# Performance work log

Measured on AMD Instinct MI355X. Metric: run time of the kernel, lower is better.

The kernel has to match this reference:

```python
import jax, jax.numpy as jnp
import numpy as np

N_NODES = 50000
N_EDGES = 800000
IN_CH = 128
HIDDEN = 64
LATENT = 64
OUT_CH = 128
N_GRAPHS = 500
NEG_SLOPE = 0.2


def _gat_layer(x, src, dst, W, a_src, a_dst, b, n_nodes):
    """PyG GATConv (heads=1, concat=True, add_self_loops=True, edge_dim=None)."""
    h = x @ W  # [N, F]
    loops = jnp.arange(n_nodes)
    s = jnp.concatenate([src, loops])  # source (j) of each edge incl. self loops
    d = jnp.concatenate([dst, loops])  # destination (i)
    score_src = h @ a_src  # [N]
    score_dst = h @ a_dst  # [N]
    alpha = jax.nn.leaky_relu(score_src[s] + score_dst[d], NEG_SLOPE)  # [E+N]
    # softmax grouped by destination node
    amax = jax.ops.segment_max(alpha, d, num_segments=n_nodes)
    e = jnp.exp(alpha - amax[d])
    denom = jax.ops.segment_sum(e, d, num_segments=n_nodes)
    coef = e / (denom[d] + 1e-16)
    out = jax.ops.segment_sum(h[s] * coef[:, None], d, num_segments=n_nodes)
    return out + b


def setup_inputs() -> dict:
    key = jax.random.key(0)
    ks = jax.random.split(key, 24)
    g = lambda k, shape, fan: jax.random.normal(k, shape, jnp.float32) * (1.0 / np.sqrt(fan))
    inp = {
        "x": jax.random.normal(ks[0], (N_NODES, IN_CH), jnp.float32),
        "edge_index": jax.random.randint(ks[1], (2, N_EDGES), 0, N_NODES, dtype=jnp.int64),
        "batch": jnp.sort(jax.random.randint(ks[2], (N_NODES,), 0, N_GRAPHS, dtype=jnp.int64)),
        "edge_attr": jax.random.normal(ks[3], (N_EDGES, 3), jnp.float32),
        # conv1 (GATConv in->hidden)
        "W1": g(ks[4], (IN_CH, HIDDEN), IN_CH),
        "a_src1": g(ks[5], (HIDDEN,), HIDDEN),
        "a_dst1": g(ks[6], (HIDDEN,), HIDDEN),
        "b1": jnp.zeros((HIDDEN,), jnp.float32),
        # conv2 (GATConv hidden->latent)
        "W2": g(ks[7], (HIDDEN, LATENT), HIDDEN),
        "a_src2": g(ks[8], (LATENT,), LATENT),
        "a_dst2": g(ks[9], (LATENT,), LATENT),
        "b2": jnp.zeros((LATENT,), jnp.float32),
        # encoder linear
        "lin_W": g(ks[10], (LATENT, LATENT), LATENT),
        "lin_b": jnp.zeros((LATENT,), jnp.float32),
        # decoder x_mlp
        "xm_W1": g(ks[11], (LATENT, HIDDEN), LATENT),
        "xm_b1": jnp.zeros((HIDDEN,), jnp.float32),
        "xm_W2": g(ks[12], (HIDDEN, OUT_CH), HIDDEN),
        "xm_b2": jnp.zeros((OUT_CH,), jnp.float32),
        # decoder edge_mlp
        "em_W1": g(ks[13], (LATENT, HIDDEN), LATENT),
        "em_b1": jnp.zeros((HIDDEN,), jnp.float32),
        "em_W2": g(ks[14], (HIDDEN, 3), HIDDEN),
        "em_b2": jnp.zeros((3,), jnp.float32),
    }
    return inp


def reference(x, edge_index, batch, edge_attr,
              W1, a_src1, a_dst1, b1,
              W2, a_src2, a_dst2, b2,
              lin_W, lin_b,
              xm_W1, xm_b1, xm_W2, xm_b2,
              em_W1, em_b1, em_W2, em_b2):
    src, dst = edge_index[0], edge_index[1]
    n = x.shape[0]
    # Encoder (eval mode: dropout is identity; edge_attr unused since edge_dim=None)
    h = _gat_layer(x, src, dst, W1, a_src1, a_dst1, b1, n)
    h = jax.nn.relu(h)
    z = _gat_layer(h, src, dst, W2, a_src2, a_dst2, b2, n)
    z = z @ lin_W + lin_b
    # global_mean_pool over batch ids
    sums = jax.ops.segment_sum(z, batch, num_segments=N_GRAPHS)
    counts = jax.ops.segment_sum(jnp.ones((n,), z.dtype), batch, num_segments=N_GRAPHS)
    graph_embedding = sums / jnp.maximum(counts, 1.0)[:, None]
    # MLP decoders
    x_hat = jax.nn.relu(z @ xm_W1 + xm_b1) @ xm_W2 + xm_b2
    e_hat = jax.nn.relu(z @ em_W1 + em_b1) @ em_W2 + em_b2
    return (x_hat, e_hat, z, graph_embedding)
```

## Files before the change

kernel.cpp:

```cpp
#include <hip/hip_runtime.h>
#include <hip/hip_bf16.h>
#include <cstring>

#define N_NODES 50000
#define N_EDGES 800000
#define IN_CH 128
#define NG 500
#define OUT_ELEMS 9782000
#define NBUCK 196
#define GEMMB 3125
#define DECB 3125

using bf16 = __hip_bfloat16;
typedef unsigned short u16;
typedef unsigned int u32;
typedef long long i64;
typedef unsigned long long u64;

__device__ __forceinline__ float b2f(bf16 v) { return __bfloat162float(v); }
__device__ __forceinline__ float tofl(float v) { return v; }
__device__ __forceinline__ float tofl(bf16 v) { return __bfloat162float(v); }
__device__ __forceinline__ float ldflt(const void* p, int i, int f32) {
  return f32 ? ((const float*)p)[i] : b2f(((const bf16*)p)[i]);
}
__device__ __forceinline__ int ldedge(const void* p, int i, int is64) {
  return is64 ? (int)((const i64*)p)[i] : ((const int*)p)[i];
}
__device__ __forceinline__ float sane(float v) {
  if (!isfinite(v)) return 0.f;
  return fminf(fmaxf(v, -65504.f), 65504.f);
}
__device__ __forceinline__ float lrelu(float x) { return x > 0.f ? x : 0.2f * x; }
__device__ __forceinline__ float bflo(u32 u) { return __uint_as_float(u << 16); }
__device__ __forceinline__ float bfhi(u32 u) { return __uint_as_float(u & 0xffff0000u); }

__device__ __forceinline__ float wsum(float v) {
#pragma unroll
  for (int o = 32; o > 0; o >>= 1) v += __shfl_xor(v, o, 64);
  return v;
}


__global__ void fillsig_kernel(float* __restrict__ out, int n, float v) {
  int i = blockIdx.x * 256 + threadIdx.x;
  if (i < n) out[i] = v;
}

#define BCHUNK 4096

__global__ __launch_bounds__(256) void hist196_kernel(const void* __restrict__ ei,
                                                      const u16* __restrict__ xb,
                                                      int* __restrict__ bpart,
                                                      int* __restrict__ fl) {
  int bid = blockIdx.x, tid = threadIdx.x;
  __shared__ int cs;
  __shared__ int hist[NBUCK];
  if (bid < NBUCK) {
    if (tid == 0) cs = 0;
    if (tid < NBUCK) hist[tid] = 0;
    __syncthreads();
    const int* e32 = (const int*)ei;
    atomicAdd(&cs, (e32[2 * tid + 1] == 0) ? 1 : 0);
    __syncthreads();
    int is64 = cs > 128;
    int base = bid * BCHUNK;
#pragma unroll
    for (int k = 0; k < 16; ++k) {
      int e = base + k * 256 + tid;
      if (e < N_EDGES) {
        unsigned d = (unsigned)ldedge(ei, N_EDGES + e, is64);
        if (d < N_NODES) atomicAdd(&hist[d >> 8], 1);
      }
    }
    __syncthreads();
    if (tid < NBUCK) bpart[bid * 256 + tid] = hist[tid];
    return;
  }
  if (tid == 0) cs = 0;
  __syncthreads();
  int cnt = 0;
  if (bid == NBUCK) {
#pragma unroll 4
    for (int k = 0; k < 32; ++k) {
      int i = tid + 256 * k;
      u16 u = xb[2 * i];
      int e = (u >> 7) & 0xFF;
      if (e != 0 && (e < 90 || e > 150)) ++cnt;
    }
  } else {
    const int* e32 = (const int*)ei;
#pragma unroll 4
    for (int k = 0; k < 32; ++k) {
      int i = tid + 256 * k;
      if (e32[2 * i + 1] == 0) ++cnt;
    }
  }
  atomicAdd(&cs, cnt);
  __syncthreads();
  if (tid == 0) fl[bid == NBUCK ? 7 : 6] = cs;
}

__global__ __launch_bounds__(256) void scan196_kernel(const int* __restrict__ bpart,
                                                      int* __restrict__ bcur,
                                                      int* __restrict__ bstart,
                                                      int* __restrict__ offs) {
  __shared__ int sm[256];
  int t = threadIdx.x;
  int sum = 0;
  if (t < NBUCK)
    for (int b = 0; b < NBUCK; ++b) sum += bpart[b * 256 + t];
  sm[t] = (t < NBUCK) ? sum : 0;
  __syncthreads();
  for (int off = 1; off < 256; off <<= 1) {
    int add = (t >= off) ? sm[t - off] : 0;
    __syncthreads();
    sm[t] += add;
    __syncthreads();
  }
  if (t < NBUCK) {
    int start = sm[t] - sum;
    bcur[t] = start;
    bstart[t] = start;
  }
  if (t == 255) {
    bstart[NBUCK] = sm[255];
    offs[N_NODES] = sm[255];
  }
}

template <int FIN, typename FT>
__device__ void gemm16_compute(float (&xl)[16][FIN], const void* Wv, const void* asv,
                               const void* adv, bf16* __restrict__ h, float* __restrict__ ss,
                               float* __restrict__ sd, int rbase) {
  const FT* W = (const FT*)Wv;
  const FT* as_ = (const FT*)asv;
  const FT* ad_ = (const FT*)adv;
  int lane = threadIdx.x & 63, w = threadIdx.x >> 6;
  float a_s = tofl(as_[lane]), a_d = tofl(ad_[lane]);
  int r0 = w * 4;
  float acc0 = 0.f, acc1 = 0.f, acc2 = 0.f, acc3 = 0.f;
  for (int k = 0; k < FIN; ++k) {
    float wk = tofl(W[k * 64 + lane]);
    acc0 = fmaf(xl[r0 + 0][k], wk, acc0);
    acc1 = fmaf(xl[r0 + 1][k], wk, acc1);
    acc2 = fmaf(xl[r0 + 2][k], wk, acc2);
    acc3 = fmaf(xl[r0 + 3][k], wk, acc3);
  }
  float acc[4] = {sane(acc0), sane(acc1), sane(acc2), sane(acc3)};
#pragma unroll
  for (int j = 0; j < 4; ++j) {
    int g = rbase + r0 + j;
    h[g * 64 + lane] = __float2bfloat16(acc[j]);
    float vs = wsum(acc[j] * a_s);
    float vd = wsum(acc[j] * a_d);
    if (lane == 0) { ss[g] = sane(vs); sd[g] = sane(vd); }
  }
}

__global__ __launch_bounds__(256) void bucket_gemm_kernel(
    const void* __restrict__ ei, int* __restrict__ bcur, u64* __restrict__ tmp,
    const void* __restrict__ xin, const void* __restrict__ W, const void* __restrict__ asrc,
    const void* __restrict__ adst, const int* __restrict__ fl, bf16* __restrict__ h,
    float* __restrict__ ss, float* __restrict__ sd) {
  __shared__ int hist[NBUCK], run[NBUCK], gbase[NBUCK];
  __shared__ float xl[16][IN_CH];
  int bid = blockIdx.x, tid = threadIdx.x;
  int is64 = fl[6] > 4000;
  int wf = fl[7] > 2000;
  if (bid < NBUCK) {
    if (tid < NBUCK) { hist[tid] = 0; run[tid] = 0; }
    __syncthreads();
    int base = bid * BCHUNK;
#pragma unroll
    for (int k = 0; k < 16; ++k) {
      int e = base + k * 256 + tid;
      if (e < N_EDGES) {
        unsigned d = (unsigned)ldedge(ei, N_EDGES + e, is64);
        if (d < N_NODES) atomicAdd(&hist[d >> 8], 1);
      }
    }
    __syncthreads();
    if (tid < NBUCK) {
      int hh = hist[tid];
      gbase[tid] = hh ? atomicAdd(&bcur[tid], hh) : 0;
    }
    __syncthreads();
#pragma unroll
    for (int k = 0; k < 16; ++k) {
      int e = base + k * 256 + tid;
      if (e < N_EDGES) {
        unsigned d = (unsigned)ldedge(ei, N_EDGES + e, is64);
        if (d < N_NODES) {
          unsigned s = (unsigned)ldedge(ei, e, is64);
          if (s >= N_NODES) s = 0;
          int pos = gbase[d >> 8] + atomicAdd(&run[d >> 8], 1);
          if ((unsigned)pos < N_EDGES) tmp[pos] = ((u64)s << 32) | (u64)d;
        }
      }
    }
    return;
  }
  int rbase = (bid - NBUCK) * 16;
  for (int i = tid; i < 16 * IN_CH; i += 256) {
    int rr = i / IN_CH, cc = i % IN_CH;
    xl[rr][cc] = ldflt(xin, (rbase + rr) * IN_CH + cc, wf);
  }
  __syncthreads();
  if (wf)
    gemm16_compute<IN_CH, float>(xl, W, asrc, adst, h, ss, sd, rbase);
  else
    gemm16_compute<IN_CH, bf16>(xl, W, asrc, adst, h, ss, sd, rbase);
}

__global__ __launch_bounds__(1024) void scatter2b_kernel(const u64* __restrict__ tmp,
                                                         const int* __restrict__ bstart,
                                                         int* __restrict__ offs,
                                                         int* __restrict__ csr) {
  __shared__ int lcnt[256], lex[256], lcur[256];
  int b = blockIdx.x;
  int tid = threadIdx.x;
  if (tid < 256) { lcnt[tid] = 0; lcur[tid] = 0; }
  __syncthreads();
  int nodelo = b << 8;
  int beg = bstart[b], end = bstart[b + 1];
  beg = max(0, min(beg, N_EDGES));
  end = max(beg, min(end, N_EDGES));
  for (int i = beg + tid; i < end; i += 1024) {
    int d = (int)(tmp[i] & 0xFFFFFFFFu);
    unsigned li = (unsigned)(d - nodelo);
    if (li < 256) atomicAdd(&lcnt[li], 1);
  }
  __syncthreads();
  if (tid < 256) lex[tid] = lcnt[tid];
  __syncthreads();
  for (int off = 1; off < 256; off <<= 1) {
    int add = (tid < 256 && tid >= off) ? lex[tid - off] : 0;
    __syncthreads();
    if (tid < 256) lex[tid] += add;
    __syncthreads();
  }
  if (tid < 256) {
    int ex = lex[tid] - lcnt[tid];
    lex[tid] = ex;
    int node = nodelo + tid;
    if (node < N_NODES) offs[node] = beg + ex;
  }
  __syncthreads();
  for (int i = beg + tid; i < end; i += 1024) {
    u64 v = tmp[i];
    int d = (int)(v & 0xFFFFFFFFu);
    int s = (int)(v >> 32);
    unsigned li = (unsigned)(d - nodelo);
    if (li < 256) {
      int pos = beg + lex[li] + atomicAdd(&lcur[li], 1);
      if ((unsigned)pos < N_EDGES) csr[pos] = s;
    }
  }
}

__device__ __forceinline__ float2 agg_node2(const bf16* __restrict__ h,
                                            const float* __restrict__ ss,
                                            const float* __restrict__ sd,
                                            const int* __restrict__ offs,
                                            const int* __restrict__ csr, int d, int lane) {
  int hl = lane & 31;
  int hbase = lane & 32;
  float sdd = sd[d];
  int beg = offs[d], end = offs[d + 1];
  beg = max(0, min(beg, N_EDGES));
  end = max(beg, min(end, N_EDGES));
  float wself = __expf(fminf(lrelu(ss[d] + sdd), 60.f));
  u32 uself = ((const u32*)h)[d * 32 + hl];
  float2 acc;
  acc.x = bflo(uself) * wself;
  acc.y = bfhi(uself) * wself;
  float dpart = (hl == 0) ? wself : 0.f;
  for (int cb = beg; cb < end; cb += 32) {
    int j = cb + hl;
    int s = 0;
    float wv = 0.f;
    if (j < end) {
      s = csr[j];
      s = ((unsigned)s < N_NODES) ? s : 0;
      wv = __expf(fminf(lrelu(ss[s] + sdd), 60.f));
    }
    dpart += wv;
    int cnt = min(32, end - cb);
    for (int t0 = 0; t0 < cnt; t0 += 16) {
      u32 hv[16];
#pragma unroll
      for (int q = 0; q < 16; ++q) {
        int sq = __shfl(s, hbase + t0 + q, 64);
        hv[q] = ((const u32*)h)[sq * 32 + hl];
      }
#pragma unroll
      for (int q = 0; q < 16; ++q) {
        float wq = __shfl(wv, hbase + t0 + q, 64);
        acc.x = fmaf(bflo(hv[q]), wq, acc.x);
        acc.y = fmaf(bfhi(hv[q]), wq, acc.y);
      }
    }
  }
#pragma unroll
  for (int o = 16; o > 0; o >>= 1) dpart += __shfl_xor(dpart, o, 64);
  float den = dpart + 1e-16f;
  acc.x = acc.x / den;
  acc.y = acc.y / den;
  return acc;
}

template <typename FT>
__device__ void gemm2_compute(float (&xl)[8][64], int r0, const void* Wv, const void* asv,
                              const void* adv, bf16* __restrict__ h, float* __restrict__ ss,
                              float* __restrict__ sd, int rbase) {
  const FT* W = (const FT*)Wv;
  const FT* as_ = (const FT*)asv;
  const FT* ad_ = (const FT*)adv;
  int lane = threadIdx.x & 63;
  float a_s = tofl(as_[lane]), a_d = tofl(ad_[lane]);
  float acc0 = 0.f, acc1 = 0.f;
  for (int k = 0; k < 64; ++k) {
    float wk = tofl(W[k * 64 + lane]);
    acc0 = fmaf(xl[r0 + 0][k], wk, acc0);
    acc1 = fmaf(xl[r0 + 1][k], wk, acc1);
  }
  float acc[2] = {sane(acc0), sane(acc1)};
#pragma unroll
  for (int j = 0; j < 2; ++j) {
    int g = rbase + r0 + j;
    h[g * 64 + lane] = __float2bfloat16(acc[j]);
    float vs = wsum(acc[j] * a_s);
    float vd = wsum(acc[j] * a_d);
    if (lane == 0) { ss[g] = sane(vs); sd[g] = sane(vd); }
  }
}

template <typename FT>
__device__ void lin2_compute(float (&xl)[8][64], int r0, const void* Wv, const void* bv,
                             float* __restrict__ zio, int rbase) {
  const FT* W = (const FT*)Wv;
  const FT* b = (const FT*)bv;
  int lane = threadIdx.x & 63;
  float bl = tofl(b[lane]);
  float acc0 = bl, acc1 = bl;
  for (int k = 0; k < 64; ++k) {
    float wk = tofl(W[k * 64 + lane]);
    acc0 = fmaf(xl[r0 + 0][k], wk, acc0);
    acc1 = fmaf(xl[r0 + 1][k], wk, acc1);
  }
  float acc[2] = {sane(acc0), sane(acc1)};
#pragma unroll
  for (int j = 0; j < 2; ++j) zio[(rbase + r0 + j) * 64 + lane] = acc[j];
}

__global__ __launch_bounds__(256) void agg_gemm_kernel(
    const bf16* __restrict__ hL, const float* __restrict__ ssL, const float* __restrict__ sdL,
    const int* __restrict__ offs, const int* __restrict__ csr, const void* __restrict__ bias,
    const int* __restrict__ fl, const void* __restrict__ W2, const void* __restrict__ as2,
    const void* __restrict__ ad2, bf16* __restrict__ hOut, float* __restrict__ ssOut,
    float* __restrict__ sdOut) {
  __shared__ float o1l[8][64];
  int wf = fl[7] > 2000;
  int lane = threadIdx.x & 63, w = threadIdx.x >> 6;
  int hl = lane & 31, half = lane >> 5;
  int rbase = blockIdx.x * 8;
  int d = rbase + 2 * w + half;
  float2 r = agg_node2(hL, ssL, sdL, offs, csr, d, lane);
  float blx = ldflt(bias, 2 * hl, wf), bly = ldflt(bias, 2 * hl + 1, wf);
  o1l[2 * w + half][2 * hl] = sane(fmaxf(r.x + blx, 0.f));
  o1l[2 * w + half][2 * hl + 1] = sane(fmaxf(r.y + bly, 0.f));
  __syncthreads();
  if (wf)
    gemm2_compute<float>(o1l, 2 * w, W2, as2, ad2, hOut, ssOut, sdOut, rbase);
  else
    gemm2_compute<bf16>(o1l, 2 * w, W2, as2, ad2, hOut, ssOut, sdOut, rbase);
}

__global__ __launch_bounds__(256) void agg_lin_kernel(
    const bf16* __restrict__ hL, const float* __restrict__ ssL, const float* __restrict__ sdL,
    const int* __restrict__ offs, const int* __restrict__ csr, const void* __restrict__ bias,
    const int* __restrict__ fl, const void* __restrict__ linW, const void* __restrict__ linb,
    float* __restrict__ zreg) {
  __shared__ float o2l[8][64];
  int wf = fl[7] > 2000;
  int lane = threadIdx.x & 63, w = threadIdx.x >> 6;
  int hl = lane & 31, half = lane >> 5;
  int rbase = blockIdx.x * 8;
  int d = rbase + 2 * w + half;
  float2 r = agg_node2(hL, ssL, sdL, offs, csr, d, lane);
  float blx = ldflt(bias, 2 * hl, wf), bly = ldflt(bias, 2 * hl + 1, wf);
  o2l[2 * w + half][2 * hl] = sane(r.x + blx);
  o2l[2 * w + half][2 * hl + 1] = sane(r.y + bly);
  __syncthreads();
  if (wf)
    lin2_compute<float>(o2l, 2 * w, linW, linb, zreg, rbase);
  else
    lin2_compute<bf16>(o2l, 2 * w, linW, linb, zreg, rbase);
}

template <typename FT>
__device__ void dec16_compute(float (&zl)[16][64], float (&t1x)[16][64], float (&t1e)[16][65],
                              float (&W2l)[192], const void* xW1v, const void* xb1v,
                              const void* xW2v, const void* xb2v, const void* eW1v,
                              const void* eb1v, const void* eb2v, float* __restrict__ xout,
                              float* __restrict__ eout, int rbase) {
  const FT* xW1 = (const FT*)xW1v;
  const FT* xb1 = (const FT*)xb1v;
  const FT* xW2 = (const FT*)xW2v;
  const FT* xb2 = (const FT*)xb2v;
  const FT* eW1 = (const FT*)eW1v;
  const FT* eb1 = (const FT*)eb1v;
  const FT* eb2 = (const FT*)eb2v;
  int lane = threadIdx.x & 63, w = threadIdx.x >> 6;
  int r0 = w * 4;
  {
    float bx = tofl(xb1[lane]), be = tofl(eb1[lane]);
    float x0 = bx, x1 = bx, x2 = bx, x3 = bx;
    float e0 = be, e1 = be, e2 = be, e3 = be;
    for (int k = 0; k < 64; ++k) {
      float z0 = zl[r0 + 0][k], z1 = zl[r0 + 1][k];
      float z2 = zl[r0 + 2][k], z3 = zl[r0 + 3][k];
      float wx = tofl(xW1[k * 64 + lane]);
      float we = tofl(eW1[k * 64 + lane]);
      x0 = fmaf(z0, wx, x0);
      x1 = fmaf(z1, wx, x1);
      x2 = fmaf(z2, wx, x2);
      x3 = fmaf(z3, wx, x3);
      e0 = fmaf(z0, we, e0);
      e1 = fmaf(z1, we, e1);
      e2 = fmaf(z2, we, e2);
      e3 = fmaf(z3, we, e3);
    }
    t1x[r0 + 0][lane] = fmaxf(x0, 0.f);
    t1x[r0 + 1][lane] = fmaxf(x1, 0.f);
    t1x[r0 + 2][lane] = fmaxf(x2, 0.f);
    t1x[r0 + 3][lane] = fmaxf(x3, 0.f);
    t1e[r0 + 0][lane] = fmaxf(e0, 0.f);
    t1e[r0 + 1][lane] = fmaxf(e1, 0.f);
    t1e[r0 + 2][lane] = fmaxf(e2, 0.f);
    t1e[r0 + 3][lane] = fmaxf(e3, 0.f);
  }
  {
    float b2a = tofl(xb2[lane]), b2b = tofl(xb2[64 + lane]);
    float a0[4] = {b2a, b2a, b2a, b2a};
    float a1[4] = {b2b, b2b, b2b, b2b};
    for (int k = 0; k < 64; ++k) {
      float wa = tofl(xW2[k * 128 + lane]);
      float wb = tofl(xW2[k * 128 + 64 + lane]);
#pragma unroll
      for (int j = 0; j < 4; ++j) {
        float tv = t1x[r0 + j][k];
        a0[j] = fmaf(tv, wa, a0[j]);
        a1[j] = fmaf(tv, wb, a1[j]);
      }
    }
#pragma unroll
    for (int j = 0; j < 4; ++j) {
      int g = rbase + r0 + j;
      xout[g * 128 + lane] = sane(a0[j]);
      xout[g * 128 + 64 + lane] = sane(a1[j]);
    }
  }
  {
    int j = lane >> 4, c = lane & 15;
    if (c < 3) {
      int row = r0 + j;
      float acc = tofl(eb2[c]);
#pragma unroll 4
      for (int k = 0; k < 64; ++k) acc = fmaf(t1e[row][k], W2l[k * 3 + c], acc);
      eout[(rbase + row) * 3 + c] = sane(acc);
    }
  }
}

__global__ __launch_bounds__(256) void dec_pool_kernel(
    const float* __restrict__ z, const void* __restrict__ xmW1, const void* __restrict__ xmb1,
    const void* __restrict__ xmW2, const void* __restrict__ xmb2, const void* __restrict__ emW1,
    const void* __restrict__ emb1, const void* __restrict__ emW2, const void* __restrict__ emb2,
    const void* __restrict__ batch, const int* __restrict__ fl, float* __restrict__ xout,
    float* __restrict__ eout, float* __restrict__ emb) {
  __shared__ float zl[16][64];
  __shared__ float t1x[16][64];
  __shared__ float t1e[16][65];
  __shared__ float W2l[192];
  int tid = threadIdx.x;
  if (blockIdx.x < NG) {
    float(&sm)[4][64] = *reinterpret_cast<float(*)[4][64]>(&zl[0][0]);
    int* bounds = (int*)&t1x[0][0];
    int g = blockIdx.x;
    int lane = tid & 63, w = tid >> 6;
    int is64 = fl[6] > 4000;
    if (tid < 2) {
      int target = g + tid;
      int lo = 0, hi = N_NODES;
      while (lo < hi) {
        int mid = (lo + hi) >> 1;
        if (ldedge(batch, mid, is64) < target) lo = mid + 1; else hi = mid;
      }
      bounds[tid] = lo;
    }
    __syncthreads();
    int beg = bounds[0], end = bounds[1];
    float acc = 0.f;
    for (int r = beg + w; r < end; r += 4) acc += z[r * 64 + lane];
    sm[w][lane] = acc;
    __syncthreads();
    if (w == 0) {
      float v = sm[0][lane] + sm[1][lane] + sm[2][lane] + sm[3][lane];
      float cnt = (float)max(end - beg, 1);
      emb[g * 64 + lane] = sane(v / cnt);
    }
    return;
  }
  int wf = fl[7] > 2000;
  int rbase = (blockIdx.x - NG) * 16;
  for (int i = tid; i < 1024; i += 256) zl[i >> 6][i & 63] = z[rbase * 64 + i];
  if (tid < 192) W2l[tid] = wf ? ((const float*)emW2)[tid] : b2f(((const bf16*)emW2)[tid]);
  __syncthreads();
  if (wf)
    dec16_compute<float>(zl, t1x, t1e, W2l, xmW1, xmb1, xmW2, xmb2, emW1, emb1, emb2,
                         xout, eout, rbase);
  else
    dec16_compute<bf16>(zl, t1x, t1e, W2l, xmW1, xmb1, xmW2, xmb2, emW1, emb1, emb2,
                        xout, eout, rbase);
}

extern "C" void kernel_launch(void* const* d_in, const int* in_sizes, int n_in,
                              void* d_out, int out_size, void* d_ws, size_t ws_size,
                              hipStream_t stream) {
  float* outf = (float*)d_out;
  if (out_size != OUT_ELEMS) {
    float sig = 2048.0f + fminf((float)out_size * 1e-4f, 999.f);
    fillsig_kernel<<<(out_size + 255) / 256, 256, 0, stream>>>(outf, out_size, sig);
    return;
  }
  if (n_in < 22 || in_sizes[0] != N_NODES * IN_CH || in_sizes[1] != 2 * N_EDGES) {
    fillsig_kernel<<<(out_size + 255) / 256, 256, 0, stream>>>(outf, out_size, 5000.f);
    return;
  }

  const void* x = d_in[0];
  const void* ei = d_in[1];
  const void* batch = d_in[2];
  const void* W1 = d_in[4];
  const void* as1 = d_in[5];
  const void* ad1 = d_in[6];
  const void* b1 = d_in[7];
  const void* W2 = d_in[8];
  const void* as2 = d_in[9];
  const void* ad2 = d_in[10];
  const void* b2 = d_in[11];
  const void* linW = d_in[12];
  const void* linb = d_in[13];
  const void* xmW1 = d_in[14];
  const void* xmb1 = d_in[15];
  const void* xmW2 = d_in[16];
  const void* xmb2 = d_in[17];
  const void* emW1 = d_in[18];
  const void* emb1 = d_in[19];
  const void* emW2 = d_in[20];
  const void* emb2 = d_in[21];

  float* xhat = outf;
  float* ehat = outf + 6400000;
  float* zreg = outf + 6550000;
  float* emb = outf + 9750000;

  bool usews = ws_size >= (size_t)17100000;
  char* base = usews ? (char*)d_ws : (char*)d_out;
  int* bpart = (int*)(base + 0);
  int* offs = (int*)(base + 400000);
  int* bcur = (int*)(base + 600016);
  int* bstart = (int*)(base + 600816);
  int* flags = (int*)(base + 601616);
  float* ssb = (float*)(base + 601728);
  float* sdb = (float*)(base + 801728);
  int* csr = (int*)(base + 1001728);
  bf16* hbuf = (bf16*)(base + 4201728);
  u64* tmp = (u64*)(base + 10601728);
  float* ss2 = (float*)(base + 0);
  float* sd2 = (float*)(base + 200000);
  bf16* hbuf2 = (bf16*)(base + 10601728);

  int err = 0, idx = 0;
  (void)hipGetLastError();
#define CK()                                                                       \
  do {                                                                             \
    ++idx;                                                                         \
    hipError_t e_ = hipGetLastError();                                             \
    if (e_ != hipSuccess && err == 0) err = 8192 + idx * 256 + ((int)e_ & 3) * 64; \
  } while (0)

  hist196_kernel<<<NBUCK + 2, 256, 0, stream>>>(ei, (const u16*)x, bpart, flags); CK();
  scan196_kernel<<<1, 256, 0, stream>>>(bpart, bcur, bstart, offs); CK();
  bucket_gemm_kernel<<<NBUCK + GEMMB, 256, 0, stream>>>(
      ei, bcur, tmp, x, W1, as1, ad1, flags, hbuf, ssb, sdb); CK();
  scatter2b_kernel<<<NBUCK, 1024, 0, stream>>>(tmp, bstart, offs, csr); CK();
  agg_gemm_kernel<<<N_NODES / 8, 256, 0, stream>>>(hbuf, ssb, sdb, offs, csr, b1, flags,
                                                   W2, as2, ad2, hbuf2, ss2, sd2); CK();
  agg_lin_kernel<<<N_NODES / 8, 256, 0, stream>>>(hbuf2, ss2, sd2, offs, csr, b2, flags,
                                                  linW, linb, zreg); CK();
  dec_pool_kernel<<<NG + DECB, 256, 0, stream>>>(zreg, xmW1, xmb1, xmW2, xmb2,
                                                 emW1, emb1, emW2, emb2, batch, flags,
                                                 xhat, ehat, emb); CK();
#undef CK

  if (err != 0) {
    static float s_sent;
    s_sent = (float)err;
    (void)hipMemcpyAsync(d_out, &s_sent, 4, hipMemcpyHostToDevice, stream);
  }
}
```

Before: 305.7 us.

## Replace histogram+scan CSR build with fixed-capacity bucket slots and packed edges

Removes the separate histogram and prefix-scan kernels by giving each destination bucket a fixed-capacity region (BCAP slots), so bucketing only needs an atomic counter per bucket, and folds the dtype-detection flags into the bucket/GEMM kernel. Edge entries are packed into 32-bit words (source shifted by 8, low destination byte) instead of 64-bit pairs, halving temp traffic. The CSR becomes padded per bucket, with explicit per-node end offsets used by the aggregation kernels. This drops two launches and one full edge pass. The cost is a larger workspace and silent truncation if any bucket exceeds its capacity.

```diff
diff --git a/kernel.cpp b/kernel.cpp
--- a/kernel.cpp
+++ b/kernel.cpp
@@ -8,6 +8,8 @@
 #define NG 500
 #define OUT_ELEMS 9782000
 #define NBUCK 196
+#define BCAP 8192
+#define CSRCAP (NBUCK * BCAP)
 #define GEMMB 3125
 #define DECB 3125
 
@@ -46,87 +48,12 @@
   if (i < n) out[i] = v;
 }
 
+__global__ void zero_kernel(int* __restrict__ p, int n) {
+  int i = threadIdx.x;
+  if (i < n) p[i] = 0;
+}
+
 #define BCHUNK 4096
-
-__global__ __launch_bounds__(256) void hist196_kernel(const void* __restrict__ ei,
-                                                      const u16* __restrict__ xb,
-                                                      int* __restrict__ bpart,
-                                                      int* __restrict__ fl) {
-  int bid = blockIdx.x, tid = threadIdx.x;
-  __shared__ int cs;
-  __shared__ int hist[NBUCK];
-  if (bid < NBUCK) {
-    if (tid == 0) cs = 0;
-    if (tid < NBUCK) hist[tid] = 0;
-    __syncthreads();
-    const int* e32 = (const int*)ei;
-    atomicAdd(&cs, (e32[2 * tid + 1] == 0) ? 1 : 0);
-    __syncthreads();
-    int is64 = cs > 128;
-    int base = bid * BCHUNK;
-#pragma unroll
-    for (int k = 0; k < 16; ++k) {
-      int e = base + k * 256 + tid;
-      if (e < N_EDGES) {
-        unsigned d = (unsigned)ldedge(ei, N_EDGES + e, is64);
-        if (d < N_NODES) atomicAdd(&hist[d >> 8], 1);
-      }
-    }
-    __syncthreads();
-    if (tid < NBUCK) bpart[bid * 256 + tid] = hist[tid];
-    return;
-  }
-  if (tid == 0) cs = 0;
-  __syncthreads();
-  int cnt = 0;
-  if (bid == NBUCK) {
-#pragma unroll 4
-    for (int k = 0; k < 32; ++k) {
-      int i = tid + 256 * k;
-      u16 u = xb[2 * i];
-      int e = (u >> 7) & 0xFF;
-      if (e != 0 && (e < 90 || e > 150)) ++cnt;
-    }
-  } else {
-    const int* e32 = (const int*)ei;
-#pragma unroll 4
-    for (int k = 0; k < 32; ++k) {
-      int i = tid + 256 * k;
-      if (e32[2 * i + 1] == 0) ++cnt;
-    }
-  }
-  atomicAdd(&cs, cnt);
-  __syncthreads();
-  if (tid == 0) fl[bid == NBUCK ? 7 : 6] = cs;
-}
-
-__global__ __launch_bounds__(256) void scan196_kernel(const int* __restrict__ bpart,
-                                                      int* __restrict__ bcur,
-                                                      int* __restrict__ bstart,
-                                                      int* __restrict__ offs) {
-  __shared__ int sm[256];
-  int t = threadIdx.x;
-  int sum = 0;
-  if (t < NBUCK)
-    for (int b = 0; b < NBUCK; ++b) sum += bpart[b * 256 + t];
-  sm[t] = (t < NBUCK) ? sum : 0;
-  __syncthreads();
-  for (int off = 1; off < 256; off <<= 1) {
-    int add = (t >= off) ? sm[t - off] : 0;
-    __syncthreads();
-    sm[t] += add;
-    __syncthreads();
-  }
-  if (t < NBUCK) {
-    int start = sm[t] - sum;
-    bcur[t] = start;
-    bstart[t] = start;
-  }
-  if (t == 255) {
-    bstart[NBUCK] = sm[255];
-    offs[N_NODES] = sm[255];
-  }
-}
 
 template <int FIN, typename FT>
 __device__ void gemm16_compute(float (&xl)[16][FIN], const void* Wv, const void* asv,
@@ -158,18 +85,22 @@
 }
 
 __global__ __launch_bounds__(256) void bucket_gemm_kernel(
-    const void* __restrict__ ei, int* __restrict__ bcur, u64* __restrict__ tmp,
+    const void* __restrict__ ei, int* __restrict__ bcnt, u32* __restrict__ tmp,
     const void* __restrict__ xin, const void* __restrict__ W, const void* __restrict__ asrc,
-    const void* __restrict__ adst, const int* __restrict__ fl, bf16* __restrict__ h,
+    const void* __restrict__ adst, int* __restrict__ fl, bf16* __restrict__ h,
     float* __restrict__ ss, float* __restrict__ sd) {
   __shared__ int hist[NBUCK], run[NBUCK], gbase[NBUCK];
   __shared__ float xl[16][IN_CH];
+  __shared__ int cs;
   int bid = blockIdx.x, tid = threadIdx.x;
-  int is64 = fl[6] > 4000;
-  int wf = fl[7] > 2000;
   if (bid < NBUCK) {
+    if (tid == 0) cs = 0;
     if (tid < NBUCK) { hist[tid] = 0; run[tid] = 0; }
     __syncthreads();
+    const int* e32 = (const int*)ei;
+    atomicAdd(&cs, (e32[2 * tid + 1] == 0) ? 1 : 0);
+    __syncthreads();
+    int is64 = cs > 128;
     int base = bid * BCHUNK;
 #pragma unroll
     for (int k = 0; k < 16; ++k) {
@@ -182,7 +113,7 @@
     __syncthreads();
     if (tid < NBUCK) {
       int hh = hist[tid];
-      gbase[tid] = hh ? atomicAdd(&bcur[tid], hh) : 0;
+      gbase[tid] = hh ? atomicAdd(&bcnt[tid], hh) : 0;
     }
     __syncthreads();
 #pragma unroll
@@ -193,14 +124,51 @@
         if (d < N_NODES) {
           unsigned s = (unsigned)ldedge(ei, e, is64);
           if (s >= N_NODES) s = 0;
-          int pos = gbase[d >> 8] + atomicAdd(&run[d >> 8], 1);
-          if ((unsigned)pos < N_EDGES) tmp[pos] = ((u64)s << 32) | (u64)d;
+          int t = d >> 8;
+          int pl = gbase[t] + atomicAdd(&run[t], 1);
+          if (pl < BCAP) tmp[t * BCAP + pl] = (s << 8) | (d & 255u);
         }
       }
     }
     return;
   }
-  int rbase = (bid - NBUCK) * 16;
+  if (bid < NBUCK + 2) {
+    if (tid == 0) cs = 0;
+    __syncthreads();
+    int cnt = 0;
+    if (bid == NBUCK) {
+      const u16* xb = (const u16*)xin;
+#pragma unroll 4
+      for (int k = 0; k < 32; ++k) {
+        int i = tid + 256 * k;
+        u16 u = xb[2 * i];
+        int e = (u >> 7) & 0xFF;
+        if (e != 0 && (e < 90 || e > 150)) ++cnt;
+      }
+    } else {
+      const int* e32 = (const int*)ei;
+#pragma unroll 4
+      for (int k = 0; k < 32; ++k) {
+        int i = tid + 256 * k;
+        if (e32[2 * i + 1] == 0) ++cnt;
+      }
+    }
+    atomicAdd(&cs, cnt);
+    __syncthreads();
+    if (tid == 0) fl[bid == NBUCK ? 7 : 6] = cs;
+    return;
+  }
+  if (tid == 0) cs = 0;
+  __syncthreads();
+  {
+    const u16* xb = (const u16*)xin;
+    u16 u = xb[2 * tid];
+    int e = (u >> 7) & 0xFF;
+    atomicAdd(&cs, (e != 0 && (e < 90 || e > 150)) ? 1 : 0);
+  }
+  __syncthreads();
+  int wf = cs > 64;
+  int rbase = (bid - NBUCK - 2) * 16;
   for (int i = tid; i < 16 * IN_CH; i += 256) {
     int rr = i / IN_CH, cc = i % IN_CH;
     xl[rr][cc] = ldflt(xin, (rbase + rr) * IN_CH + cc, wf);
@@ -212,9 +180,10 @@
     gemm16_compute<IN_CH, bf16>(xl, W, asrc, adst, h, ss, sd, rbase);
 }
 
-__global__ __launch_bounds__(1024) void scatter2b_kernel(const u64* __restrict__ tmp,
-                                                         const int* __restrict__ bstart,
+__global__ __launch_bounds__(1024) void scatter2c_kernel(const u32* __restrict__ tmp,
+                                                         const int* __restrict__ bcnt,
                                                          int* __restrict__ offs,
+                                                         int* __restrict__ ends,
                                                          int* __restrict__ csr) {
   __shared__ int lcnt[256], lex[256], lcur[256];
   int b = blockIdx.x;
@@ -222,13 +191,11 @@
   if (tid < 256) { lcnt[tid] = 0; lcur[tid] = 0; }
   __syncthreads();
   int nodelo = b << 8;
-  int beg = bstart[b], end = bstart[b + 1];
-  beg = max(0, min(beg, N_EDGES));
-  end = max(beg, min(end, N_EDGES));
-  for (int i = beg + tid; i < end; i += 1024) {
-    int d = (int)(tmp[i] & 0xFFFFFFFFu);
-    unsigned li = (unsigned)(d - nodelo);
-    if (li < 256) atomicAdd(&lcnt[li], 1);
+  int cnt = min(bcnt[b], BCAP);
+  int tbase = b * BCAP;
+  for (int i = tid; i < cnt; i += 1024) {
+    int li = (int)(tmp[tbase + i] & 255u);
+    atomicAdd(&lcnt[li], 1);
   }
   __syncthreads();
   if (tid < 256) lex[tid] = lcnt[tid];
@@ -243,18 +210,18 @@
     int ex = lex[tid] - lcnt[tid];
     lex[tid] = ex;
     int node = nodelo + tid;
-    if (node < N_NODES) offs[node] = beg + ex;
-  }
-  __syncthreads();
-  for (int i = beg + tid; i < end; i += 1024) {
-    u64 v = tmp[i];
-    int d = (int)(v & 0xFFFFFFFFu);
-    int s = (int)(v >> 32);
-    unsigned li = (unsigned)(d - nodelo);
-    if (li < 256) {
-      int pos = beg + lex[li] + atomicAdd(&lcur[li], 1);
-      if ((unsigned)pos < N_EDGES) csr[pos] = s;
-    }
+    if (node < N_NODES) {
+      offs[node] = tbase + ex;
+      ends[node] = tbase + ex + lcnt[tid];
+    }
+  }
+  __syncthreads();
+  for (int i = tid; i < cnt; i += 1024) {
+    u32 v = tmp[tbase + i];
+    int li = (int)(v & 255u);
+    int s = (int)(v >> 8);
+    int pos = tbase + lex[li] + atomicAdd(&lcur[li], 1);
+    if (pos < CSRCAP) csr[pos] = s;
   }
 }
 
@@ -262,13 +229,14 @@
                                             const float* __restrict__ ss,
                                             const float* __restrict__ sd,
                                             const int* __restrict__ offs,
+                                            const int* __restrict__ ends,
                                             const int* __restrict__ csr, int d, int lane) {
   int hl = lane & 31;
   int hbase = lane & 32;
   float sdd = sd[d];
-  int beg = offs[d], end = offs[d + 1];
-  beg = max(0, min(beg, N_EDGES));
-  end = max(beg, min(end, N_EDGES));
+  int beg = offs[d], end = ends[d];
+  beg = max(0, min(beg, CSRCAP));
+  end = max(beg, min(end, CSRCAP));
   float wself = __expf(fminf(lrelu(ss[d] + sdd), 60.f));
   u32 uself = ((const u32*)h)[d * 32 + hl];
   float2 acc;
@@ -355,17 +323,17 @@
 
 __global__ __launch_bounds__(256) void agg_gemm_kernel(
     const bf16* __restrict__ hL, const float* __restrict__ ssL, const float* __restrict__ sdL,
-    const int* __restrict__ offs, const int* __restrict__ csr, const void* __restrict__ bias,
-    const int* __restrict__ fl, const void* __restrict__ W2, const void* __restrict__ as2,
-    const void* __restrict__ ad2, bf16* __restrict__ hOut, float* __restrict__ ssOut,
-    float* __restrict__ sdOut) {
+    const int* __restrict__ offs, const int* __restrict__ ends, const int* __restrict__ csr,
+    const void* __restrict__ bias, const int* __restrict__ fl, const void* __restrict__ W2,
+    const void* __restrict__ as2, const void* __restrict__ ad2, bf16* __restrict__ hOut,
+    float* __restrict__ ssOut, float* __restrict__ sdOut) {
   __shared__ float o1l[8][64];
   int wf = fl[7] > 2000;
   int lane = threadIdx.x & 63, w = threadIdx.x >> 6;
   int hl = lane & 31, half = lane >> 5;
   int rbase = blockIdx.x * 8;
   int d = rbase + 2 * w + half;
-  float2 r = agg_node2(hL, ssL, sdL, offs, csr, d, lane);
+  float2 r = agg_node2(hL, ssL, sdL, offs, ends, csr, d, lane);
   float blx = ldflt(bias, 2 * hl, wf), bly = ldflt(bias, 2 * hl + 1, wf);
   o1l[2 * w + half][2 * hl] = sane(fmaxf(r.x + blx, 0.f));
   o1l[2 * w + half][2 * hl + 1] = sane(fmaxf(r.y + bly, 0.f));
@@ -378,16 +346,16 @@
 
 __global__ __launch_bounds__(256) void agg_lin_kernel(
     const bf16* __restrict__ hL, const float* __restrict__ ssL, const float* __restrict__ sdL,
-    const int* __restrict__ offs, const int* __restrict__ csr, const void* __restrict__ bias,
-    const int* __restrict__ fl, const void* __restrict__ linW, const void* __restrict__ linb,
-    float* __restrict__ zreg) {
+    const int* __restrict__ offs, const int* __restrict__ ends, const int* __restrict__ csr,
+    const void* __restrict__ bias, const int* __restrict__ fl, const void* __restrict__ linW,
+    const void* __restrict__ linb, float* __restrict__ zreg) {
   __shared__ float o2l[8][64];
   int wf = fl[7] > 2000;
   int lane = threadIdx.x & 63, w = threadIdx.x >> 6;
   int hl = lane & 31, half = lane >> 5;
   int rbase = blockIdx.x * 8;
   int d = rbase + 2 * w + half;
-  float2 r = agg_node2(hL, ssL, sdL, offs, csr, d, lane);
+  float2 r = agg_node2(hL, ssL, sdL, offs, ends, csr, d, lane);
   float blx = ldflt(bias, 2 * hl, wf), bly = ldflt(bias, 2 * hl + 1, wf);
   o2l[2 * w + half][2 * hl] = sane(r.x + blx);
   o2l[2 * w + half][2 * hl + 1] = sane(r.y + bly);
@@ -566,21 +534,20 @@
   float* zreg = outf + 6550000;
   float* emb = outf + 9750000;
 
-  bool usews = ws_size >= (size_t)17100000;
+  bool usews = ws_size >= (size_t)20500000;
   char* base = usews ? (char*)d_ws : (char*)d_out;
-  int* bpart = (int*)(base + 0);
-  int* offs = (int*)(base + 400000);
-  int* bcur = (int*)(base + 600016);
-  int* bstart = (int*)(base + 600816);
-  int* flags = (int*)(base + 601616);
-  float* ssb = (float*)(base + 601728);
-  float* sdb = (float*)(base + 801728);
-  int* csr = (int*)(base + 1001728);
-  bf16* hbuf = (bf16*)(base + 4201728);
-  u64* tmp = (u64*)(base + 10601728);
-  float* ss2 = (float*)(base + 0);
-  float* sd2 = (float*)(base + 200000);
-  bf16* hbuf2 = (bf16*)(base + 10601728);
+  int* bcnt = (int*)(base + 0);
+  int* flags = (int*)(base + 800);
+  int* offs = (int*)(base + 1024);
+  int* ends = (int*)(base + 201024);
+  float* ssb = (float*)(base + 401024);
+  float* sdb = (float*)(base + 601024);
+  int* csr = (int*)(base + 801024);
+  bf16* hbuf = (bf16*)(base + 7223552);
+  u32* tmp = (u32*)(base + 13623552);
+  float* ss2 = (float*)(base + 13623552);
+  float* sd2 = (float*)(base + 13823552);
+  bf16* hbuf2 = (bf16*)(base + 14023552);
 
   int err = 0, idx = 0;
   (void)hipGetLastError();
@@ -591,15 +558,14 @@
     if (e_ != hipSuccess && err == 0) err = 8192 + idx * 256 + ((int)e_ & 3) * 64; \
   } while (0)
 
-  hist196_kernel<<<NBUCK + 2, 256, 0, stream>>>(ei, (const u16*)x, bpart, flags); CK();
-  scan196_kernel<<<1, 256, 0, stream>>>(bpart, bcur, bstart, offs); CK();
-  bucket_gemm_kernel<<<NBUCK + GEMMB, 256, 0, stream>>>(
-      ei, bcur, tmp, x, W1, as1, ad1, flags, hbuf, ssb, sdb); CK();
-  scatter2b_kernel<<<NBUCK, 1024, 0, stream>>>(tmp, bstart, offs, csr); CK();
-  agg_gemm_kernel<<<N_NODES / 8, 256, 0, stream>>>(hbuf, ssb, sdb, offs, csr, b1, flags,
-                                                   W2, as2, ad2, hbuf2, ss2, sd2); CK();
-  agg_lin_kernel<<<N_NODES / 8, 256, 0, stream>>>(hbuf2, ss2, sd2, offs, csr, b2, flags,
-                                                  linW, linb, zreg); CK();
+  zero_kernel<<<1, 256, 0, stream>>>(bcnt, 200); CK();
+  bucket_gemm_kernel<<<NBUCK + 2 + GEMMB, 256, 0, stream>>>(
+      ei, bcnt, tmp, x, W1, as1, ad1, flags, hbuf, ssb, sdb); CK();
+  scatter2c_kernel<<<NBUCK, 1024, 0, stream>>>(tmp, bcnt, offs, ends, csr); CK();
+  agg_gemm_kernel<<<N_NODES / 8, 256, 0, stream>>>(hbuf, ssb, sdb, offs, ends, csr, b1,
+                                                   flags, W2, as2, ad2, hbuf2, ss2, sd2); CK();
+  agg_lin_kernel<<<N_NODES / 8, 256, 0, stream>>>(hbuf2, ss2, sd2, offs, ends, csr, b2,
+                                                  flags, linW, linb, zreg); CK();
   dec_pool_kernel<<<NG + DECB, 256, 0, stream>>>(zreg, xmW1, xmb1, xmW2, xmb2,
                                                  emW1, emb1, emW2, emb2, batch, flags,
                                                  xhat, ehat, emb); CK();
```

After: 287.8 us. 5.8% less time.
